# Kernel optimization log

Measured on AMD Instinct MI355X. Metric: run time of the kernel, lower is better.

Reference implementation:

```python
import jax, jax.numpy as jnp
import numpy as np

TOKENS = 8192
IN_F = 4096
OUT_F = 4096
QMAX = 127.0  # int8 symmetric quant range
EPS = 1e-8


def setup_inputs() -> dict:
    key = jax.random.key(0)
    k1, k2, k3, k4 = jax.random.split(key, 4)
    x = jax.random.normal(k1, (TOKENS, IN_F), dtype=jnp.float32)
    # Pre-quantized int8 weight [out_features, in_features]
    weight_q = jax.random.randint(k2, (OUT_F, IN_F), -127, 128, dtype=jnp.int8)
    # Per-output-channel weight scales (realistic small magnitudes)
    weight_scale = jax.random.uniform(k3, (OUT_F,), dtype=jnp.float32) * 0.01 + 1e-3
    bias = jax.random.normal(k4, (OUT_F,), dtype=jnp.float32)
    return {"x": x, "weight_q": weight_q, "weight_scale": weight_scale, "bias": bias}


def reference(x, weight_q, weight_scale, bias):
    # Dynamic per-token symmetric int8 activation quantization
    absmax = jnp.max(jnp.abs(x), axis=-1, keepdims=True)           # [T, 1]
    x_scale = jnp.maximum(absmax, EPS) / QMAX                      # [T, 1]
    x_q = jnp.clip(jnp.round(x / x_scale), -QMAX, QMAX).astype(jnp.int8)
    acc = jax.lax.dot_general(
        x_q, weight_q,
        dimension_numbers=(((1,), (1,)), ((), ())),
        preferred_element_type=jnp.int32,
    )
    # Inline dequant: per-token activation scale * per-channel weight scale
    out = acc.astype(jnp.float32) * x_scale * weight_scale[None, :]
    out = out + bias[None, :]
    return out
```

## Files before the change

kernel.cpp:

```cpp
#include <hip/hip_runtime.h>
#include <cstdint>
#include <cstddef>

#define TOKENS 8192
#define IN_F   4096
#define OUT_F  4096
#define QMAXF  127.0f
#define EPSF   1e-8f

typedef int i32x4  __attribute__((ext_vector_type(4)));
typedef int i32x16 __attribute__((ext_vector_type(16)));

#define BKB 64
#define NT  (IN_F / BKB)
#define ABYTES 16384
#define BUFB   24576

__device__ __forceinline__ void gload16(const void* g, void* l) {
    __builtin_amdgcn_global_load_lds(
        (const __attribute__((address_space(1))) void*)g,
        (__attribute__((address_space(3))) void*)l,
        16, 0, 0);
}

__device__ __forceinline__ int quant1(float v, float inv) {
    int q = (int)rintf(v * inv);
    q = q > 127 ? 127 : q;
    q = q < -127 ? -127 : q;
    return q;
}

__device__ __forceinline__ unsigned int pack4i(int a, int b, int c, int d) {
    return (unsigned int)(a & 255) | ((unsigned int)(b & 255) << 8) |
           ((unsigned int)(c & 255) << 16) | ((unsigned int)(d & 255) << 24);
}

__global__ __launch_bounds__(256) void quant_x_kernel(const float* __restrict__ x,
                                                      signed char* __restrict__ xq,
                                                      float* __restrict__ xscale) {
    const int t   = blockIdx.x;
    const int tid = threadIdx.x;
    const float* xr = x + (size_t)t * IN_F + tid * 16;

    float4 v[4];
    float am = 0.0f;
#pragma unroll
    for (int i = 0; i < 4; ++i) {
        v[i] = ((const float4*)xr)[i];
        am = fmaxf(am, fmaxf(fmaxf(fabsf(v[i].x), fabsf(v[i].y)),
                             fmaxf(fabsf(v[i].z), fabsf(v[i].w))));
    }
#pragma unroll
    for (int off = 32; off >= 1; off >>= 1)
        am = fmaxf(am, __shfl_xor(am, off));

    __shared__ float wmax[4];
    const int wid = tid >> 6, lane = tid & 63;
    if (lane == 0) wmax[wid] = am;
    __syncthreads();
    am = fmaxf(fmaxf(wmax[0], wmax[1]), fmaxf(wmax[2], wmax[3]));

    const float s   = fmaxf(am, EPSF) / QMAXF;
    const float inv = QMAXF / fmaxf(am, EPSF);
    if (tid == 0) xscale[t] = s;

    unsigned int w[4];
#pragma unroll
    for (int i = 0; i < 4; ++i) {
        w[i] = pack4i(quant1(v[i].x, inv), quant1(v[i].y, inv),
                      quant1(v[i].z, inv), quant1(v[i].w, inv));
    }
    *(uint4*)(xq + (size_t)t * IN_F + tid * 16) = make_uint4(w[0], w[1], w[2], w[3]);
}

__global__ __launch_bounds__(256) void pack_w_kernel(const int* __restrict__ w,
                                                     signed char* __restrict__ wq) {
    const size_t idx = (size_t)blockIdx.x * 256 + threadIdx.x;
    const int4* src = (const int4*)w + idx * 4;
    unsigned int o[4];
#pragma unroll
    for (int i = 0; i < 4; ++i) {
        int4 u = src[i];
        o[i] = pack4i(u.x, u.y, u.z, u.w);
    }
    ((uint4*)wq)[idx] = make_uint4(o[0], o[1], o[2], o[3]);
}

__global__ __launch_bounds__(256, 2) void gemm_kernel(const signed char* __restrict__ xq,
                                                      const signed char* __restrict__ wq,
                                                      const float* __restrict__ xscale,
                                                      const float* __restrict__ wscale,
                                                      const float* __restrict__ bias,
                                                      float* __restrict__ out) {
    __shared__ __align__(16) char lds[2 * BUFB];

    const int tid  = threadIdx.x;
    const int wid  = tid >> 6;
    const int lane = tid & 63;
    const int wr   = wid >> 1;
    const int wc   = wid & 1;

    const int bid = blockIdx.x;
    const int swz = (bid & 7) * 128 + (bid >> 3);
    const int bm0 = (swz >> 5) * 256;
    const int bn0 = (swz & 31) * 128;

    const int srow = ((tid >> 6) << 4) + (tid & 15);
    const int scol = ((tid >> 4) & 3) * 16;
    const signed char* pA = xq + (size_t)(bm0 + srow) * IN_F + scol;
    const signed char* pB = wq + (size_t)(bn0 + srow) * IN_F + scol;
    const int ldst = tid * 16;

    const int l31 = lane & 31, hi = lane >> 5;
    int a_off[4][2], b_off[2][2];
#pragma unroll
    for (int m = 0; m < 4; ++m) {
        const int win = wr * 8 + m * 2 + (l31 >> 4);
#pragma unroll
        for (int ks = 0; ks < 2; ++ks)
            a_off[m][ks] = win * 1024 + (ks * 2 + hi) * 256 + (l31 & 15) * 16;
    }
#pragma unroll
    for (int n = 0; n < 2; ++n) {
        const int win = wc * 4 + n * 2 + (l31 >> 4);
#pragma unroll
        for (int ks = 0; ks < 2; ++ks)
            b_off[n][ks] = ABYTES + win * 1024 + (ks * 2 + hi) * 256 + (l31 & 15) * 16;
    }

    i32x16 acc[4][2];
#pragma unroll
    for (int m = 0; m < 4; ++m)
#pragma unroll
        for (int n = 0; n < 2; ++n)
#pragma unroll
            for (int r = 0; r < 16; ++r) acc[m][n][r] = 0;

    {
        char* S = lds;
#pragma unroll
        for (int c = 0; c < 4; ++c)
            gload16(pA + (size_t)c * 64 * IN_F, S + c * 4096 + ldst);
#pragma unroll
        for (int c = 0; c < 2; ++c)
            gload16(pB + (size_t)c * 64 * IN_F, S + ABYTES + c * 4096 + ldst);
    }
    asm volatile("s_waitcnt vmcnt(0)" ::: "memory");
    __builtin_amdgcn_s_barrier();

    for (int t = 0; t < NT; ++t) {
        const char* Ab = lds + (t & 1) * BUFB;

        if (t + 1 < NT) {
            char* S = lds + ((t + 1) & 1) * BUFB;
            const int ko = (t + 1) * BKB;
#pragma unroll
            for (int c = 0; c < 4; ++c)
                gload16(pA + (size_t)c * 64 * IN_F + ko, S + c * 4096 + ldst);
#pragma unroll
            for (int c = 0; c < 2; ++c)
                gload16(pB + (size_t)c * 64 * IN_F + ko, S + ABYTES + c * 4096 + ldst);
        }

        i32x4 b[2][2], a[4][2];
#pragma unroll
        for (int n = 0; n < 2; ++n)
#pragma unroll
            for (int ks = 0; ks < 2; ++ks)
                b[n][ks] = *(const i32x4*)(Ab + b_off[n][ks]);
#pragma unroll
        for (int m = 0; m < 4; ++m)
#pragma unroll
            for (int ks = 0; ks < 2; ++ks)
                a[m][ks] = *(const i32x4*)(Ab + a_off[m][ks]);

        __builtin_amdgcn_s_setprio(1);
#pragma unroll
        for (int m = 0; m < 4; ++m)
#pragma unroll
            for (int n = 0; n < 2; ++n)
#pragma unroll
                for (int ks = 0; ks < 2; ++ks)
                    acc[m][n] = __builtin_amdgcn_mfma_i32_32x32x32_i8(a[m][ks], b[n][ks], acc[m][n], 0, 0, 0);
        __builtin_amdgcn_s_setprio(0);

        asm volatile("s_waitcnt vmcnt(0)" ::: "memory");
        __builtin_amdgcn_s_barrier();
    }

#pragma unroll
    for (int m = 0; m < 4; ++m) {
        const int rbase = bm0 + wr * 128 + m * 32 + 4 * hi;
        float xsv[16];
#pragma unroll
        for (int r = 0; r < 16; ++r)
            xsv[r] = xscale[rbase + (r & 3) + 8 * (r >> 2)];
#pragma unroll
        for (int n = 0; n < 2; ++n) {
            const int col = bn0 + wc * 64 + n * 32 + l31;
            const float wsc = wscale[col];
            const float bv  = bias[col];
#pragma unroll
            for (int r = 0; r < 16; ++r) {
                const int row = rbase + (r & 3) + 8 * (r >> 2);
                out[(size_t)row * OUT_F + col] = (float)acc[m][n][r] * xsv[r] * wsc + bv;
            }
        }
    }
}

extern "C" void kernel_launch(void* const* d_in, const int* in_sizes, int n_in,
                              void* d_out, int out_size, void* d_ws, size_t ws_size,
                              hipStream_t stream) {
    const float* x      = (const float*)d_in[0];
    const int*   w      = (const int*)d_in[1];
    const float* wscale = (const float*)d_in[2];
    const float* bias   = (const float*)d_in[3];
    float* out = (float*)d_out;

    char* ws = (char*)d_ws;
    signed char* xq  = (signed char*)ws;
    signed char* wq8 = (signed char*)(ws + (size_t)TOKENS * IN_F);
    float* xscale    = (float*)(ws + (size_t)TOKENS * IN_F + (size_t)OUT_F * IN_F);

    quant_x_kernel<<<TOKENS, 256, 0, stream>>>(x, xq, xscale);
    pack_w_kernel<<<(OUT_F * (IN_F / 16)) / 256, 256, 0, stream>>>(w, wq8);
    gemm_kernel<<<(TOKENS / 256) * (OUT_F / 128), 256, 0, stream>>>(
        xq, wq8, xscale, wscale, bias, out);
}
```

Measured before the change: 246.1 us.

## Enlarge GEMM tile to 256x256 with per-wave private LDS buffers, no barriers

The block tile grows from 256x128 to 256x256, so each wave now owns a 128x128 sub-tile with a 4x4 accumulator grid. Each wave stages its own A and B slices into a private double-buffered LDS region of 32 KB, which removes block-wide barriers in favour of per-wave vmcnt waits. This raises MFMA work per loaded byte. It also needs 128 KB of dynamic LDS and many more accumulator registers, which limits occupancy to one block per CU. A and B data shared between waves is no longer reused through LDS, so each wave loads its own copy, and the grid has half as many blocks.

```diff
diff --git a/kernel.cpp b/kernel.cpp
--- a/kernel.cpp
+++ b/kernel.cpp
@@ -13,8 +13,9 @@
 
 #define BKB 64
 #define NT  (IN_F / BKB)
-#define ABYTES 16384
-#define BUFB   24576
+#define WAVE_LDS  32768
+#define BUF_LDS   16384
+#define LDS_TOTAL 131072
 
 __device__ __forceinline__ void gload16(const void* g, void* l) {
     __builtin_amdgcn_global_load_lds(
@@ -86,13 +87,13 @@
     ((uint4*)wq)[idx] = make_uint4(o[0], o[1], o[2], o[3]);
 }
 
-__global__ __launch_bounds__(256, 2) void gemm_kernel(const signed char* __restrict__ xq,
+__global__ __launch_bounds__(256, 1) void gemm_kernel(const signed char* __restrict__ xq,
                                                       const signed char* __restrict__ wq,
                                                       const float* __restrict__ xscale,
                                                       const float* __restrict__ wscale,
                                                       const float* __restrict__ bias,
                                                       float* __restrict__ out) {
-    __shared__ __align__(16) char lds[2 * BUFB];
+    extern __shared__ __align__(16) char lds[];
 
     const int tid  = threadIdx.x;
     const int wid  = tid >> 6;
@@ -101,91 +102,83 @@
     const int wc   = wid & 1;
 
     const int bid = blockIdx.x;
-    const int swz = (bid & 7) * 128 + (bid >> 3);
-    const int bm0 = (swz >> 5) * 256;
-    const int bn0 = (swz & 31) * 128;
-
-    const int srow = ((tid >> 6) << 4) + (tid & 15);
-    const int scol = ((tid >> 4) & 3) * 16;
-    const signed char* pA = xq + (size_t)(bm0 + srow) * IN_F + scol;
-    const signed char* pB = wq + (size_t)(bn0 + srow) * IN_F + scol;
-    const int ldst = tid * 16;
+    const int swz = (bid & 7) * 64 + (bid >> 3);
+    const int bm0 = (swz >> 4) * 256;
+    const int bn0 = (swz & 15) * 256;
+
+    char* wbase = lds + wid * WAVE_LDS;
+
+    const int l15 = lane & 15, lg = lane >> 4;
+    const signed char* pA = xq + (size_t)(bm0 + wr * 128 + l15) * IN_F + lg * 16;
+    const signed char* pB = wq + (size_t)(bn0 + wc * 128 + l15) * IN_F + lg * 16;
+    const int dst = lane * 16;
 
     const int l31 = lane & 31, hi = lane >> 5;
-    int a_off[4][2], b_off[2][2];
+    int a_off[4][2], b_off[4][2];
 #pragma unroll
     for (int m = 0; m < 4; ++m) {
-        const int win = wr * 8 + m * 2 + (l31 >> 4);
+        const int win = m * 2 + (l31 >> 4);
 #pragma unroll
         for (int ks = 0; ks < 2; ++ks)
             a_off[m][ks] = win * 1024 + (ks * 2 + hi) * 256 + (l31 & 15) * 16;
     }
 #pragma unroll
-    for (int n = 0; n < 2; ++n) {
-        const int win = wc * 4 + n * 2 + (l31 >> 4);
+    for (int n = 0; n < 4; ++n) {
+        const int win = n * 2 + (l31 >> 4);
 #pragma unroll
         for (int ks = 0; ks < 2; ++ks)
-            b_off[n][ks] = ABYTES + win * 1024 + (ks * 2 + hi) * 256 + (l31 & 15) * 16;
-    }
-
-    i32x16 acc[4][2];
+            b_off[n][ks] = 8192 + win * 1024 + (ks * 2 + hi) * 256 + (l31 & 15) * 16;
+    }
+
+    i32x16 acc[4][4];
 #pragma unroll
     for (int m = 0; m < 4; ++m)
 #pragma unroll
-        for (int n = 0; n < 2; ++n)
+        for (int n = 0; n < 4; ++n)
 #pragma unroll
             for (int r = 0; r < 16; ++r) acc[m][n][r] = 0;
 
-    {
-        char* S = lds;
-#pragma unroll
-        for (int c = 0; c < 4; ++c)
-            gload16(pA + (size_t)c * 64 * IN_F, S + c * 4096 + ldst);
-#pragma unroll
-        for (int c = 0; c < 2; ++c)
-            gload16(pB + (size_t)c * 64 * IN_F, S + ABYTES + c * 4096 + ldst);
-    }
-    asm volatile("s_waitcnt vmcnt(0)" ::: "memory");
-    __builtin_amdgcn_s_barrier();
-
-    for (int t = 0; t < NT; ++t) {
-        const char* Ab = lds + (t & 1) * BUFB;
-
-        if (t + 1 < NT) {
-            char* S = lds + ((t + 1) & 1) * BUFB;
-            const int ko = (t + 1) * BKB;
-#pragma unroll
-            for (int c = 0; c < 4; ++c)
-                gload16(pA + (size_t)c * 64 * IN_F + ko, S + c * 4096 + ldst);
-#pragma unroll
-            for (int c = 0; c < 2; ++c)
-                gload16(pB + (size_t)c * 64 * IN_F + ko, S + ABYTES + c * 4096 + ldst);
+#pragma unroll
+    for (int c = 0; c < 8; ++c)
+        gload16(pA + (size_t)c * 16 * IN_F, wbase + c * 1024 + dst);
+#pragma unroll
+    for (int c = 0; c < 8; ++c)
+        gload16(pB + (size_t)c * 16 * IN_F, wbase + 8192 + c * 1024 + dst);
+
+    for (int k = 0; k < NT; ++k) {
+        asm volatile("s_waitcnt vmcnt(0)" ::: "memory");
+        __builtin_amdgcn_sched_barrier(0);
+
+        const char* buf = wbase + (k & 1) * BUF_LDS;
+
+        if (k + 1 < NT) {
+            char* nb = wbase + ((k + 1) & 1) * BUF_LDS;
+            const int ko = (k + 1) * BKB;
+#pragma unroll
+            for (int c = 0; c < 8; ++c)
+                gload16(pA + (size_t)c * 16 * IN_F + ko, nb + c * 1024 + dst);
+#pragma unroll
+            for (int c = 0; c < 8; ++c)
+                gload16(pB + (size_t)c * 16 * IN_F + ko, nb + 8192 + c * 1024 + dst);
         }
 
-        i32x4 b[2][2], a[4][2];
-#pragma unroll
-        for (int n = 0; n < 2; ++n)
-#pragma unroll
-            for (int ks = 0; ks < 2; ++ks)
-                b[n][ks] = *(const i32x4*)(Ab + b_off[n][ks]);
-#pragma unroll
-        for (int m = 0; m < 4; ++m)
-#pragma unroll
-            for (int ks = 0; ks < 2; ++ks)
-                a[m][ks] = *(const i32x4*)(Ab + a_off[m][ks]);
-
-        __builtin_amdgcn_s_setprio(1);
-#pragma unroll
-        for (int m = 0; m < 4; ++m)
-#pragma unroll
-            for (int n = 0; n < 2; ++n)
-#pragma unroll
-                for (int ks = 0; ks < 2; ++ks)
+        i32x4 a[4][2], b[4][2];
+#pragma unroll
+        for (int m = 0; m < 4; ++m) a[m][0] = *(const i32x4*)(buf + a_off[m][0]);
+#pragma unroll
+        for (int n = 0; n < 4; ++n) b[n][0] = *(const i32x4*)(buf + b_off[n][0]);
+#pragma unroll
+        for (int m = 0; m < 4; ++m) a[m][1] = *(const i32x4*)(buf + a_off[m][1]);
+#pragma unroll
+        for (int n = 0; n < 4; ++n) b[n][1] = *(const i32x4*)(buf + b_off[n][1]);
+
+#pragma unroll
+        for (int ks = 0; ks < 2; ++ks)
+#pragma unroll
+            for (int m = 0; m < 4; ++m)
+#pragma unroll
+                for (int n = 0; n < 4; ++n)
                     acc[m][n] = __builtin_amdgcn_mfma_i32_32x32x32_i8(a[m][ks], b[n][ks], acc[m][n], 0, 0, 0);
-        __builtin_amdgcn_s_setprio(0);
-
-        asm volatile("s_waitcnt vmcnt(0)" ::: "memory");
-        __builtin_amdgcn_s_barrier();
     }
 
 #pragma unroll
@@ -196,8 +189,8 @@
         for (int r = 0; r < 16; ++r)
             xsv[r] = xscale[rbase + (r & 3) + 8 * (r >> 2)];
 #pragma unroll
-        for (int n = 0; n < 2; ++n) {
-            const int col = bn0 + wc * 64 + n * 32 + l31;
+        for (int n = 0; n < 4; ++n) {
+            const int col = bn0 + wc * 128 + n * 32 + l31;
             const float wsc = wscale[col];
             const float bv  = bias[col];
 #pragma unroll
@@ -223,8 +216,11 @@
     signed char* wq8 = (signed char*)(ws + (size_t)TOKENS * IN_F);
     float* xscale    = (float*)(ws + (size_t)TOKENS * IN_F + (size_t)OUT_F * IN_F);
 
+    hipFuncSetAttribute((const void*)gemm_kernel,
+                        hipFuncAttributeMaxDynamicSharedMemorySize, LDS_TOTAL);
+
     quant_x_kernel<<<TOKENS, 256, 0, stream>>>(x, xq, xscale);
     pack_w_kernel<<<(OUT_F * (IN_F / 16)) / 256, 256, 0, stream>>>(w, wq8);
-    gemm_kernel<<<(TOKENS / 256) * (OUT_F / 128), 256, 0, stream>>>(
+    gemm_kernel<<<(TOKENS / 256) * (OUT_F / 256), 256, LDS_TOTAL, stream>>>(
         xq, wq8, xscale, wscale, bias, out);
 }
```

After: 299.6 us. 1.22x slower.

## Enlarge GEMM block tile to 256x256 with 8 waves and 128-byte K steps

Applied to the files above, without the earlier changes.

The int8 GEMM now uses 512-thread blocks, each computing a 256x256 output tile, and double-buffers 128-byte K slices in 128KB of dynamic LDS. The larger tile and deeper K step are meant to raise operand reuse per LDS load, halve global traffic per output, and halve the number of barriers per K. The trade-off is much higher LDS use, which likely limits each CU to one block and reduces latency hiding.

```diff
diff --git a/kernel.cpp b/kernel.cpp
--- a/kernel.cpp
+++ b/kernel.cpp
@@ -11,16 +11,22 @@
 typedef int i32x4  __attribute__((ext_vector_type(4)));
 typedef int i32x16 __attribute__((ext_vector_type(16)));
 
-#define BKB 64
-#define NT  (IN_F / BKB)
-#define ABYTES 16384
-#define BUFB   24576
+#define BKB 128
+#define NTT (IN_F / BKB)
+#define SLOT 65536
+#define LDS_TOTAL (2 * SLOT)
 
 __device__ __forceinline__ void gload16(const void* g, void* l) {
     __builtin_amdgcn_global_load_lds(
         (const __attribute__((address_space(1))) void*)g,
         (__attribute__((address_space(3))) void*)l,
         16, 0, 0);
+}
+
+__device__ __forceinline__ void bar() {
+    asm volatile("" ::: "memory");
+    __builtin_amdgcn_s_barrier();
+    asm volatile("" ::: "memory");
 }
 
 __device__ __forceinline__ int quant1(float v, float inv) {
@@ -86,124 +92,127 @@
     ((uint4*)wq)[idx] = make_uint4(o[0], o[1], o[2], o[3]);
 }
 
-__global__ __launch_bounds__(256, 2) void gemm_kernel(const signed char* __restrict__ xq,
+__global__ __launch_bounds__(512, 2) void gemm_kernel(const signed char* __restrict__ xq,
                                                       const signed char* __restrict__ wq,
                                                       const float* __restrict__ xscale,
                                                       const float* __restrict__ wscale,
                                                       const float* __restrict__ bias,
                                                       float* __restrict__ out) {
-    __shared__ __align__(16) char lds[2 * BUFB];
+    extern __shared__ __align__(16) char lds[];
 
     const int tid  = threadIdx.x;
     const int wid  = tid >> 6;
     const int lane = tid & 63;
-    const int wr   = wid >> 1;
-    const int wc   = wid & 1;
+    const int wr   = wid >> 2;
+    const int wc   = wid & 3;
 
     const int bid = blockIdx.x;
-    const int swz = (bid & 7) * 128 + (bid >> 3);
-    const int bm0 = (swz >> 5) * 256;
-    const int bn0 = (swz & 31) * 128;
-
-    const int srow = ((tid >> 6) << 4) + (tid & 15);
-    const int scol = ((tid >> 4) & 3) * 16;
-    const signed char* pA = xq + (size_t)(bm0 + srow) * IN_F + scol;
-    const signed char* pB = wq + (size_t)(bn0 + srow) * IN_F + scol;
+    const int swz = (bid & 7) * 64 + (bid >> 3);
+    const int bm0 = (swz >> 4) * 256;
+    const int bn0 = (swz & 15) * 256;
+
+    const int srow = ((tid >> 7) << 4) + (tid & 15);
+    const int skb  = ((tid >> 6) & 1) * 64 + (((tid >> 4) & 3) << 4);
+    const signed char* pA = xq + (size_t)(bm0 + srow) * IN_F + skb;
+    const signed char* pB = wq + (size_t)(bn0 + srow) * IN_F + skb;
     const int ldst = tid * 16;
 
     const int l31 = lane & 31, hi = lane >> 5;
-    int a_off[4][2], b_off[2][2];
-#pragma unroll
-    for (int m = 0; m < 4; ++m) {
-        const int win = wr * 8 + m * 2 + (l31 >> 4);
-#pragma unroll
-        for (int ks = 0; ks < 2; ++ks)
-            a_off[m][ks] = win * 1024 + (ks * 2 + hi) * 256 + (l31 & 15) * 16;
-    }
-#pragma unroll
-    for (int n = 0; n < 2; ++n) {
-        const int win = wc * 4 + n * 2 + (l31 >> 4);
-#pragma unroll
-        for (int ks = 0; ks < 2; ++ks)
-            b_off[n][ks] = ABYTES + win * 1024 + (ks * 2 + hi) * 256 + (l31 & 15) * 16;
+    int a_off[4][4], b_off[2][4];
+#pragma unroll
+    for (int mi = 0; mi < 4; ++mi) {
+        const int row = wr * 128 + mi * 32 + l31;
+#pragma unroll
+        for (int ks = 0; ks < 4; ++ks)
+            a_off[mi][ks] = (row >> 4) * 2048 + (ks >> 1) * 1024 +
+                            (((ks & 1) * 2 + hi) << 8) + (row & 15) * 16;
+    }
+#pragma unroll
+    for (int ni = 0; ni < 2; ++ni) {
+        const int row = wc * 64 + ni * 32 + l31;
+#pragma unroll
+        for (int ks = 0; ks < 4; ++ks)
+            b_off[ni][ks] = 32768 + (row >> 4) * 2048 + (ks >> 1) * 1024 +
+                            (((ks & 1) * 2 + hi) << 8) + (row & 15) * 16;
     }
 
     i32x16 acc[4][2];
 #pragma unroll
-    for (int m = 0; m < 4; ++m)
-#pragma unroll
-        for (int n = 0; n < 2; ++n)
-#pragma unroll
-            for (int r = 0; r < 16; ++r) acc[m][n][r] = 0;
-
-    {
-        char* S = lds;
-#pragma unroll
-        for (int c = 0; c < 4; ++c)
-            gload16(pA + (size_t)c * 64 * IN_F, S + c * 4096 + ldst);
-#pragma unroll
-        for (int c = 0; c < 2; ++c)
-            gload16(pB + (size_t)c * 64 * IN_F, S + ABYTES + c * 4096 + ldst);
-    }
+    for (int mi = 0; mi < 4; ++mi)
+#pragma unroll
+        for (int ni = 0; ni < 2; ++ni)
+#pragma unroll
+            for (int r = 0; r < 16; ++r) acc[mi][ni][r] = 0;
+
+#pragma unroll
+    for (int c = 0; c < 4; ++c)
+        gload16(pA + (size_t)c * 64 * IN_F, lds + c * 8192 + ldst);
+#pragma unroll
+    for (int c = 0; c < 4; ++c)
+        gload16(pB + (size_t)c * 64 * IN_F, lds + 32768 + c * 8192 + ldst);
     asm volatile("s_waitcnt vmcnt(0)" ::: "memory");
-    __builtin_amdgcn_s_barrier();
-
-    for (int t = 0; t < NT; ++t) {
-        const char* Ab = lds + (t & 1) * BUFB;
-
-        if (t + 1 < NT) {
-            char* S = lds + ((t + 1) & 1) * BUFB;
+    bar();
+
+    for (int t = 0; t < NTT; ++t) {
+        const char* S = lds + (t & 1) * SLOT;
+
+        if (t + 1 < NTT) {
+            char* D = lds + ((t + 1) & 1) * SLOT;
             const int ko = (t + 1) * BKB;
 #pragma unroll
             for (int c = 0; c < 4; ++c)
-                gload16(pA + (size_t)c * 64 * IN_F + ko, S + c * 4096 + ldst);
-#pragma unroll
-            for (int c = 0; c < 2; ++c)
-                gload16(pB + (size_t)c * 64 * IN_F + ko, S + ABYTES + c * 4096 + ldst);
+                gload16(pA + (size_t)c * 64 * IN_F + ko, D + c * 8192 + ldst);
+#pragma unroll
+            for (int c = 0; c < 4; ++c)
+                gload16(pB + (size_t)c * 64 * IN_F + ko, D + 32768 + c * 8192 + ldst);
         }
 
-        i32x4 b[2][2], a[4][2];
-#pragma unroll
-        for (int n = 0; n < 2; ++n)
-#pragma unroll
-            for (int ks = 0; ks < 2; ++ks)
-                b[n][ks] = *(const i32x4*)(Ab + b_off[n][ks]);
-#pragma unroll
-        for (int m = 0; m < 4; ++m)
-#pragma unroll
-            for (int ks = 0; ks < 2; ++ks)
-                a[m][ks] = *(const i32x4*)(Ab + a_off[m][ks]);
-
-        __builtin_amdgcn_s_setprio(1);
-#pragma unroll
-        for (int m = 0; m < 4; ++m)
-#pragma unroll
-            for (int n = 0; n < 2; ++n)
-#pragma unroll
-                for (int ks = 0; ks < 2; ++ks)
-                    acc[m][n] = __builtin_amdgcn_mfma_i32_32x32x32_i8(a[m][ks], b[n][ks], acc[m][n], 0, 0, 0);
-        __builtin_amdgcn_s_setprio(0);
+#pragma unroll
+        for (int kh = 0; kh < 2; ++kh) {
+            i32x4 a[4][2], b[2][2];
+#pragma unroll
+            for (int mi = 0; mi < 4; ++mi)
+#pragma unroll
+                for (int k2 = 0; k2 < 2; ++k2)
+                    a[mi][k2] = *(const i32x4*)(S + a_off[mi][kh * 2 + k2]);
+#pragma unroll
+            for (int ni = 0; ni < 2; ++ni)
+#pragma unroll
+                for (int k2 = 0; k2 < 2; ++k2)
+                    b[ni][k2] = *(const i32x4*)(S + b_off[ni][kh * 2 + k2]);
+
+            __builtin_amdgcn_s_setprio(1);
+#pragma unroll
+            for (int k2 = 0; k2 < 2; ++k2)
+#pragma unroll
+                for (int mi = 0; mi < 4; ++mi)
+#pragma unroll
+                    for (int ni = 0; ni < 2; ++ni)
+                        acc[mi][ni] = __builtin_amdgcn_mfma_i32_32x32x32_i8(
+                            a[mi][k2], b[ni][k2], acc[mi][ni], 0, 0, 0);
+            __builtin_amdgcn_s_setprio(0);
+        }
 
         asm volatile("s_waitcnt vmcnt(0)" ::: "memory");
-        __builtin_amdgcn_s_barrier();
-    }
-
-#pragma unroll
-    for (int m = 0; m < 4; ++m) {
-        const int rbase = bm0 + wr * 128 + m * 32 + 4 * hi;
+        bar();
+    }
+
+#pragma unroll
+    for (int mi = 0; mi < 4; ++mi) {
+        const int rbase = bm0 + wr * 128 + mi * 32 + 4 * hi;
         float xsv[16];
 #pragma unroll
         for (int r = 0; r < 16; ++r)
             xsv[r] = xscale[rbase + (r & 3) + 8 * (r >> 2)];
 #pragma unroll
-        for (int n = 0; n < 2; ++n) {
-            const int col = bn0 + wc * 64 + n * 32 + l31;
+        for (int ni = 0; ni < 2; ++ni) {
+            const int col = bn0 + wc * 64 + ni * 32 + l31;
             const float wsc = wscale[col];
             const float bv  = bias[col];
 #pragma unroll
             for (int r = 0; r < 16; ++r) {
                 const int row = rbase + (r & 3) + 8 * (r >> 2);
-                out[(size_t)row * OUT_F + col] = (float)acc[m][n][r] * xsv[r] * wsc + bv;
+                out[(size_t)row * OUT_F + col] = (float)acc[mi][ni][r] * xsv[r] * wsc + bv;
             }
         }
     }
@@ -223,8 +232,11 @@
     signed char* wq8 = (signed char*)(ws + (size_t)TOKENS * IN_F);
     float* xscale    = (float*)(ws + (size_t)TOKENS * IN_F + (size_t)OUT_F * IN_F);
 
+    hipFuncSetAttribute((const void*)gemm_kernel,
+                        hipFuncAttributeMaxDynamicSharedMemorySize, LDS_TOTAL);
+
     quant_x_kernel<<<TOKENS, 256, 0, stream>>>(x, xq, xscale);
     pack_w_kernel<<<(OUT_F * (IN_F / 16)) / 256, 256, 0, stream>>>(w, wq8);
-    gemm_kernel<<<(TOKENS / 256) * (OUT_F / 128), 256, 0, stream>>>(
+    gemm_kernel<<<(TOKENS / 256) * (OUT_F / 256), 512, LDS_TOTAL, stream>>>(
         xq, wq8, xscale, wscale, bias, out);
 }
```

After: 215.1 us. -12.6%, faster.
